# Performance work log

Hardware: AMD Instinct MI355X
Metric: run time of the kernel (lower is better)

## Reference

```python
import jax, jax.numpy as jnp
import numpy as np

B, T_ENC, T_DEC = 32, 512, 500
D_ENC = 512
N_MEL = 80 * 2  # mel_channels * mel_scale
K = 31          # location conv kernel size


def setup_inputs() -> dict:
    key = jax.random.key(0)
    ks = jax.random.split(key, 16)
    def w(k, shape, s=0.05):
        return jax.random.normal(k, shape, jnp.float32) * s
    z = lambda n: jnp.zeros((n,), jnp.float32)
    return {
        "encoder_out": w(ks[0], (B, T_ENC, D_ENC), 1.0),
        "mels": w(ks[1], (B, T_DEC, N_MEL), 1.0),
        "mask": jnp.zeros((B, 1, T_ENC), jnp.bool_),
        "w_pre1": w(ks[2], (256, N_MEL)), "b_pre1": z(256),
        "w_pre2": w(ks[3], (256, 256)), "b_pre2": z(256),
        "wih_a": w(ks[4], (4096, 256 + 512)), "whh_a": w(ks[5], (4096, 1024)),
        "bih_a": z(4096), "bhh_a": z(4096),
        "wq": w(ks[6], (128, 1024)), "bq": z(128),
        "wk": w(ks[7], (128, 512)), "bk": z(128),
        "conv_w": w(ks[8], (32, 2, K)), "conv_b": z(32),
        "wl": w(ks[9], (128, 32)), "bl": z(128),
        "wa": w(ks[10], (1, 128)), "ba": z(1),
        "wih_d": w(ks[11], (4096, 512 + 1024)), "whh_d": w(ks[12], (4096, 1024)),
        "bih_d": z(4096), "bhh_d": z(4096),
        "wm": w(ks[13], (N_MEL, 512 + 1024)), "bm": z(N_MEL),
        "wg": w(ks[14], (1, 512 + 1024)), "bg": z(1),
    }


def _lstm_cell(x, h, c, wih, whh, bih, bhh):
    g = x @ wih.T + bih + h @ whh.T + bhh
    i, f, gg, o = jnp.split(g, 4, axis=-1)
    c = jax.nn.sigmoid(f) * c + jax.nn.sigmoid(i) * jnp.tanh(gg)
    return jax.nn.sigmoid(o) * jnp.tanh(c), c


def _forward(encoder_out, mels, mask, w_pre1, b_pre1, w_pre2, b_pre2,
             wih_a, whh_a, bih_a, bhh_a, wq, bq, wk, bk, conv_w, conv_b,
             wl, bl, wa, ba, wih_d, whh_d, bih_d, bhh_d, wm, bm, wg, bg):
    b, t_enc, _ = encoder_out.shape
    n_mel = mels.shape[-1]
    mask1 = mask[:, 0, :]  # [B, T_enc], True = masked out
    # prepend zero frame, run prenet (ReLU MLP) over all frames at once
    mel_seq = jnp.concatenate([jnp.zeros((b, 1, n_mel), mels.dtype), mels], 1)
    pre = jax.nn.relu(mel_seq @ w_pre1.T + b_pre1)
    pre = jax.nn.relu(pre @ w_pre2.T + b_pre2)        # [B, T_dec+1, 256]
    pre = pre.transpose(1, 0, 2)                      # [T_dec+1, B, 256]
    mem_keys = encoder_out @ wk.T + bk                # [B, T_enc, 128]
    pad = K // 2

    def step(carry, mel_t):
        ctx, ah, ac, aw, awt, dh, dc = carry
        ah, ac = _lstm_cell(jnp.concatenate([mel_t, ctx], -1), ah, ac,
                            wih_a, whh_a, bih_a, bhh_a)
        query = ah @ wq.T + bq                        # [B, 128]
        fmap = jnp.stack([aw, awt], axis=1)           # [B, 2, T_enc]
        loc = jax.lax.conv_general_dilated(
            fmap, conv_w, (1,), [(pad, pad)],
            dimension_numbers=("NCH", "OIH", "NCH")) + conv_b[None, :, None]
        loc = loc.transpose(0, 2, 1) @ wl.T + bl      # [B, T_enc, 128]
        e = jnp.tanh(query[:, None, :] + mem_keys + loc) @ wa.T + ba  # [B,T_enc,1]
        e = jnp.where(mask1, -jnp.inf, e[..., 0])
        aw = jax.nn.softmax(e, -1)                    # [B, T_enc]
        awt = awt + aw
        ctx = jnp.einsum("bt,btd->bd", aw, encoder_out)
        dh, dc = _lstm_cell(jnp.concatenate([ctx, ah], -1), dh, dc,
                            wih_d, whh_d, bih_d, bhh_d)
        h = jnp.concatenate([dh, ctx], -1)            # [B, 1536]
        return (ctx, ah, ac, aw, awt, dh, dc), (h @ wm.T + bm, h @ wg.T + bg, aw)

    zf = lambda *s: jnp.zeros(s, encoder_out.dtype)
    carry0 = (zf(b, 512), zf(b, 1024), zf(b, 1024), zf(b, t_enc), zf(b, t_enc),
              zf(b, 1024), zf(b, 1024))
    _, (mels_out, gates_out, attn_out) = jax.lax.scan(step, carry0, pre)
    # mels_out [T_dec+1,B,n_mel], gates_out [T_dec+1,B,1], attn_out [T_dec+1,B,T_enc]
    return mels_out, gates_out, attn_out


def reference(encoder_out, mels, mask, w_pre1, b_pre1, w_pre2, b_pre2,
              wih_a, whh_a, bih_a, bhh_a, wq, bq, wk, bk, conv_w, conv_b,
              wl, bl, wa, ba, wih_d, whh_d, bih_d, bhh_d, wm, bm, wg, bg):
    return _forward(encoder_out, mels, mask, w_pre1, b_pre1, w_pre2, b_pre2,
                    wih_a, whh_a, bih_a, bhh_a, wq, bq, wk, bk, conv_w, conv_b,
                    wl, bl, wa, ba, wih_d, whh_d, bih_d, bhh_d, wm, bm, wg, bg)
```

## Files before the change

kernel.cpp:

```cpp
#include <hip/hip_runtime.h>
#include <hip/hip_bf16.h>


typedef __hip_bfloat16 bf16;

__device__ __forceinline__ float b2f(bf16 x){ return __bfloat162float(x); }
__device__ __forceinline__ bf16 f2b(float x){ return __float2bfloat16(x); }
__device__ __forceinline__ unsigned short f2bu(float x){
  union { bf16 h; unsigned short u; } cv; cv.h = __float2bfloat16(x); return cv.u;
}
__device__ __forceinline__ float us2f(unsigned short u){
  return __uint_as_float(((unsigned)u) << 16);
}
__device__ __forceinline__ float sig_s(float x){
  if (x > 30.f) return 1.f; if (x < -30.f) return 0.f;
  return 1.f/(1.f+__expf(-x)); }
__device__ __forceinline__ float tanh_s(float x){
  if (x > 15.f) return 1.f; if (x < -15.f) return -1.f;
  float e=__expf(2.f*x); return 1.f-2.f/(e+1.f); }

__device__ __forceinline__ float ld_cv(const float* p){
  return __hip_atomic_load(p, __ATOMIC_RELAXED, __HIP_MEMORY_SCOPE_AGENT);
}
__device__ __forceinline__ void st_cv(float* p, float v){
  __hip_atomic_store(p, v, __ATOMIC_RELAXED, __HIP_MEMORY_SCOPE_AGENT);
}

constexpr size_t S_MKT   = 32ull*128*512;
constexpr size_t OFF_MKT = 0;
constexpr size_t OFF_AC  = OFF_MKT + S_MKT;
constexpr size_t OFF_DC  = OFF_AC + 32*1024;
constexpr size_t OFF_AW  = OFF_DC + 32*1024;
constexpr size_t OFF_AWT = OFF_AW + 32*512;
constexpr size_t OFF_BARS= OFF_AWT + 32*512;
constexpr size_t OFF_XA  = OFF_BARS + 3072;
constexpr size_t ZERO_LEN = OFF_XA - OFF_AC;
constexpr size_t OFF_XD  = OFF_XA + 32*1792;
constexpr size_t OFF_GP  = OFF_XD + 32*2560;
constexpr size_t OFF_CNV = OFF_GP + 8ull*32*4096;
constexpr size_t OFF_RED = OFF_CNV + 32ull*32*512;
constexpr size_t OFF_BIASA = OFF_RED + 512;
constexpr size_t OFF_BIASD = OFF_BIASA + 4096;
constexpr size_t OFF_WQT   = OFF_BIASD + 4096;
constexpr size_t OFF_F32_END = OFF_WQT + 1024*128;

constexpr size_t OFF_PRE2B_BYTES = ((OFF_F32_END*4 + 255)/256)*256;
constexpr size_t S_PRE2B = 501ull*32*256;
constexpr size_t OFF_WAT_BYTES = ((OFF_PRE2B_BYTES + S_PRE2B*2 + 255)/256)*256;
constexpr size_t S_WAT = 1792ull*4096;
constexpr size_t OFF_WDT_BYTES = OFF_WAT_BYTES + S_WAT*2;
constexpr size_t S_WDT = 2560ull*4096;
constexpr size_t WS_NEEDED = OFF_WDT_BYTES + S_WDT*2;

constexpr int LDS_WA = 57344;
constexpr int LDS_WD = 81920;
constexpr int LDS_SCR = 23552;
constexpr int SMEM_TOTAL = LDS_WA + LDS_WD + LDS_SCR;

constexpr size_t OUT_MEL  = 0;
constexpr size_t OUT_GATE = 501ull*32*160;
constexpr size_t OUT_ATTN = OUT_GATE + 501ull*32;

__global__ void k_zero(float* __restrict__ p, int n){
  int i = blockIdx.x*256 + threadIdx.x;
  if (i < n) p[i] = 0.f;
}

__global__ void k_bias(const float* __restrict__ b1, const float* __restrict__ b2,
                       float* __restrict__ out){
  int i = blockIdx.x*256 + threadIdx.x;
  if (i < 4096) out[i] = b1[i] + b2[i];
}

__global__ __launch_bounds__(256) void k_wqT(const float* __restrict__ wq,
                                             float* __restrict__ wqT){
  int idx = blockIdx.x*256 + threadIdx.x;
  int k = idx >> 7, c = idx & 127;
  wqT[idx] = wq[(size_t)c*1024 + k];
}

__global__ __launch_bounds__(256) void k_trans(const float* __restrict__ src, int C,
    unsigned short* __restrict__ dst, int koff, int CH, int SLICE){
  __shared__ unsigned short tile[64][65];
  int r0 = blockIdx.x*64, c0 = blockIdx.y*64;
  int tx = threadIdx.x & 63, ty = threadIdx.x >> 6;
  for (int rr = ty; rr < 64; rr += 4)
    tile[rr][tx] = f2bu(src[(size_t)(r0+rr)*C + c0 + tx]);
  __syncthreads();
  for (int rr = ty; rr < 64; rr += 4){
    int k = koff + c0 + rr;
    int kcc = k / CH, kl = k - kcc*CH;
    int j = r0 + tx, jtt = j >> 7, jl = j & 127;
    dst[(size_t)(kcc*32 + jtt)*SLICE + (size_t)(kl >> 2)*512 + jl*4 + (kl & 3)] = tile[tx][rr];
  }
}

__global__ __launch_bounds__(256) void k_prenet(const float* __restrict__ mels,
    const float* __restrict__ w1, const float* __restrict__ b1,
    const float* __restrict__ w2, const float* __restrict__ b2,
    bf16* __restrict__ pre2){
  __shared__ float mel[160];
  __shared__ float x1[256];
  int b = blockIdx.x, tid = threadIdx.x;
  for (int ti = 0; ti < 8; ++ti){
    int tt = blockIdx.y*8 + ti;
    if (tt >= 501) break;
    if (tid < 160) mel[tid] = (tt == 0) ? 0.f : mels[((size_t)b*500 + (tt-1))*160 + tid];
    __syncthreads();
    float a = b1[tid];
    for (int k = 0; k < 160; ++k) a += mel[k]*w1[tid*160 + k];
    x1[tid] = fmaxf(a, 0.f);
    __syncthreads();
    float a2 = b2[tid];
    for (int k = 0; k < 256; ++k) a2 += x1[k]*w2[tid*256 + k];
    pre2[((size_t)tt*32 + b)*256 + tid] = f2b(fmaxf(a2, 0.f));
    __syncthreads();
  }
}

__global__ __launch_bounds__(128) void k_memkeys(const float* __restrict__ enc,
    const float* __restrict__ wk, const float* __restrict__ bk, float* __restrict__ mkT){
  __shared__ float er[512];
  int b = blockIdx.x, tid = threadIdx.x;
  for (int i = 0; i < 8; ++i){
    int t = blockIdx.y*8 + i;
    const float* e = enc + ((size_t)b*512 + t)*512;
    for (int k = tid; k < 512; k += 128) er[k] = e[k];
    __syncthreads();
    float a = bk[tid];
    for (int k = 0; k < 512; ++k) a += er[k]*wk[tid*512 + k];
    mkT[((size_t)b*128 + tid)*512 + t] = a;
    __syncthreads();
  }
}

__device__ __forceinline__ void gridbar(unsigned* cnt){
  asm volatile("s_waitcnt vmcnt(0) lgkmcnt(0)" ::: "memory");
  __syncthreads();
  if (threadIdx.x == 0){
    __hip_atomic_fetch_add(cnt, 1u, __ATOMIC_RELAXED, __HIP_MEMORY_SCOPE_AGENT);
    while (__hip_atomic_load(cnt, __ATOMIC_RELAXED, __HIP_MEMORY_SCOPE_AGENT) < 256u)
      __builtin_amdgcn_s_sleep(16);
  }
  __syncthreads();
}

template<int CH, int KS, int HK>
__device__ __forceinline__ void gates_phase(const unsigned short* __restrict__ smW,
    float* __restrict__ xs, const float* __restrict__ xcat,
    float* __restrict__ Gp, int jt, int kc, int tid){
  const int jl = tid & 127, bg = tid >> 7;
  float acc[8];
  #pragma unroll
  for (int i = 0; i < 8; ++i) acc[i] = 0.f;
  const int k0 = kc*CH;
  for (int h = 0; h < CH/HK; ++h){
    __syncthreads();
    for (int i = tid; i < 32*HK; i += 512){
      int b = i / HK, kk = i - b*HK;
      xs[i] = ld_cv(xcat + (size_t)b*KS + k0 + h*HK + kk);
    }
    __syncthreads();
    for (int kk = 0; kk < HK; kk += 4){
      const ushort4 w4 = *(const ushort4*)(smW + (size_t)((h*HK + kk) >> 2)*512 + jl*4);
      const float w0 = us2f(w4.x), w1 = us2f(w4.y), w2 = us2f(w4.z), w3 = us2f(w4.w);
      #pragma unroll
      for (int bb = 0; bb < 8; ++bb){
        const float4 xv = *(const float4*)&xs[(bg*8 + bb)*HK + kk];
        acc[bb] = fmaf(xv.x, w0, acc[bb]);
        acc[bb] = fmaf(xv.y, w1, acc[bb]);
        acc[bb] = fmaf(xv.z, w2, acc[bb]);
        acc[bb] = fmaf(xv.w, w3, acc[bb]);
      }
    }
  }
  float* gp = Gp + (size_t)kc*131072 + (size_t)(bg*8)*4096 + jt*128 + jl;
  #pragma unroll
  for (int bb = 0; bb < 8; ++bb) st_cv(gp + (size_t)bb*4096, acc[bb]);
}

__device__ __forceinline__ void out_proj(int wid, int lane, int t,
    const float* __restrict__ xcatD, const float* __restrict__ wm,
    const float* __restrict__ bm, const float* __restrict__ wg,
    const float* __restrict__ bg,
    float* __restrict__ melOut, float* __restrict__ gateOut, int stride){
  for (int oidx = wid; oidx < 32*161; oidx += stride){
    int b = oidx / 161, jo = oidx - b*161;
    const float* wrow = (jo < 160) ? (wm + (size_t)jo*1536) : wg;
    const float* xd = xcatD + (size_t)b*2560;
    float a = 0.f;
    for (int k = lane; k < 1536; k += 64){
      float x = (k < 1024) ? ld_cv(xd + 1536 + k) : ld_cv(xd + (k - 1024));
      a = fmaf(x, wrow[k], a);
    }
    #pragma unroll
    for (int off = 32; off; off >>= 1) a += __shfl_down(a, off, 64);
    if (lane == 0){
      if (jo < 160) melOut[((size_t)t*32 + b)*160 + jo] = a + bm[jo];
      else gateOut[t*32 + b] = a + bg[0];
    }
  }
}

__global__ __launch_bounds__(512) void k_decoder(
    const unsigned short* __restrict__ WaT, const unsigned short* __restrict__ WdT,
    const float* __restrict__ biasA, const float* __restrict__ biasD,
    const bf16* __restrict__ pre2b, const float* __restrict__ mkT,
    const float* __restrict__ enc, const unsigned char* __restrict__ mask,
    const float* __restrict__ wqT, const float* __restrict__ wl,
    const float* __restrict__ bq, const float* __restrict__ bl,
    const float* __restrict__ wa, const float* __restrict__ ba,
    const float* __restrict__ conv_w, const float* __restrict__ conv_b,
    const float* __restrict__ wm, const float* __restrict__ bm,
    const float* __restrict__ wg, const float* __restrict__ bg,
    float* __restrict__ xcatA, float* __restrict__ xcatD,
    float* __restrict__ ac, float* __restrict__ dc,
    float* __restrict__ aw, float* __restrict__ awt,
    float* __restrict__ Gp, float* __restrict__ cnv,
    float* __restrict__ redG, unsigned* __restrict__ bars,
    float* __restrict__ melOut, float* __restrict__ gateOut, float* __restrict__ attnOut)
{
  extern __shared__ __align__(16) char sm[];
  unsigned short* smWa = (unsigned short*)sm;
  unsigned short* smWd = (unsigned short*)(sm + LDS_WA);
  char* scr = sm + LDS_WA + LDS_WD;
  float* xs   = (float*)scr;
  float* s0   = (float*)scr;
  float* s1   = (float*)(scr + 640);
  float* wlS  = (float*)scr;
  float* ahS  = (float*)(scr + 16384);
  float* qpP  = (float*)(scr + 20480);
  float* sqS  = (float*)(scr + 22528);
  float* eT   = (float*)(scr + 23040);
  float* sawL = (float*)(scr + 23296);

  const int blk = blockIdx.x, tid = threadIdx.x;
  const int lane = tid & 63, wv = tid >> 6;
  const int jt = blk & 31, kc = blk >> 5;

  {
    const ushort4* sa = (const ushort4*)(WaT + (size_t)(kc*32 + jt)*28672);
    ushort4* da = (ushort4*)smWa;
    for (int i = tid; i < 7168; i += 512) da[i] = sa[i];
    const ushort4* sd = (const ushort4*)(WdT + (size_t)(kc*32 + jt)*40960);
    ushort4* dd = (ushort4*)smWd;
    for (int i = tid; i < 10240; i += 512) dd[i] = sd[i];
  }
  for (int idx = blk*512 + tid; idx < 32*1792; idx += 131072){
    int b = idx / 1792, i = idx - b*1792;
    st_cv(xcatA + idx, (i < 256) ? b2f(pre2b[b*256 + i]) : 0.f);
  }
  for (int idx = blk*512 + tid; idx < 32*2560; idx += 131072) st_cv(xcatD + idx, 0.f);

  int bi = 0;
  gridbar(bars + bi); ++bi;

  for (int t = 0; t < 501; ++t){
    gates_phase<224, 1792, 112>(smWa, xs, xcatA, Gp, jt, kc, tid);
    gridbar(bars + bi); ++bi;

    if (blk < 64){
      int idx = blk*512 + tid, b = idx >> 10, u = idx & 1023;
      float gi = biasA[u], gf = biasA[1024+u], gg = biasA[2048+u], go = biasA[3072+u];
      #pragma unroll
      for (int ci = 0; ci < 8; ++ci){
        const float* p = Gp + (size_t)ci*131072 + (size_t)b*4096 + u;
        gi += ld_cv(p); gf += ld_cv(p+1024); gg += ld_cv(p+2048); go += ld_cv(p+3072);
      }
      float cp = ac[idx];
      float cn = sig_s(gf)*cp + sig_s(gi)*tanh_s(gg);
      float hh = sig_s(go)*tanh_s(cn);
      ac[idx] = cn;
      st_cv(xcatA + (size_t)b*1792 + 768 + u, hh);
      st_cv(xcatD + (size_t)b*2560 + 512 + u, hh);
    } else if (blk < 128){
      if (t > 0)
        out_proj((blk-64)*8 + wv, lane, t-1, xcatD, wm, bm, wg, bg, melOut, gateOut, 512);
    } else {
      int cb = blk - 128, b = cb >> 2, tc = cb & 3, tbase = tc*128;
      for (int i = tid; i < 316; i += 512){
        int ch = (i >= 158), p2 = ch ? i-158 : i;
        int pos = tbase + p2 - 15;
        float v = (pos >= 0 && pos < 512)
                ? (ch ? ld_cv(awt + b*512 + pos) : ld_cv(aw + b*512 + pos)) : 0.f;
        if (ch) s1[p2] = v; else s0[p2] = v;
      }
      __syncthreads();
      int tt2 = tid & 127, oh = tid >> 7;
      float acc[8];
      #pragma unroll
      for (int o = 0; o < 8; ++o) acc[o] = 0.f;
      for (int k = 0; k < 31; ++k){
        float v0 = s0[tt2+k], v1 = s1[tt2+k];
        #pragma unroll
        for (int o = 0; o < 8; ++o){
          int oo = oh*8 + o;
          acc[o] = fmaf(conv_w[oo*62 + k], v0, fmaf(conv_w[oo*62 + 31 + k], v1, acc[o]));
        }
      }
      int tg = tbase + tt2;
      #pragma unroll
      for (int o = 0; o < 8; ++o){
        int oo = oh*8 + o;
        st_cv(cnv + ((size_t)b*32 + oo)*512 + tg, acc[o] + conv_b[oo]);
      }
    }
    gridbar(bars + bi); ++bi;

    {
      int b = blk >> 3, tt = blk & 7, t0 = tt*64;
      if (tid < 64){
        st_cv(xcatA + (size_t)b*1792 + 256 + t0 + tid, 0.f);
        st_cv(xcatD + (size_t)b*2560 + t0 + tid, 0.f);
      }
      for (int i = tid; i < 4096; i += 512) wlS[i] = wl[i];
      for (int i = tid; i < 1024; i += 512) ahS[i] = ld_cv(xcatA + (size_t)b*1792 + 768 + i);
      __syncthreads();
      {
        int c = tid & 127, kq = tid >> 7;
        const float* ap = ahS + kq*256;
        const float* wp = wqT + (size_t)(kq*256)*128 + c;
        float p = 0.f;
        for (int k = 0; k < 256; ++k) p = fmaf(ap[k], wp[(size_t)k*128], p);
        qpP[kq*128 + c] = p;
      }
      __syncthreads();
      if (tid < 128)
        sqS[tid] = qpP[tid] + qpP[128+tid] + qpP[256+tid] + qpP[384+tid] + bq[tid] + bl[tid];
      __syncthreads();
      int tl = tid & 63, cg = tid >> 6;
      float rv[32];
      {
        const float* cp2 = cnv + (size_t)b*32*512 + t0 + tl;
        #pragma unroll
        for (int o = 0; o < 32; ++o) rv[o] = ld_cv(cp2 + (size_t)o*512);
      }
      float a = 0.f;
      const float* mkb = mkT + (size_t)b*65536 + t0 + tl;
      for (int ci = 0; ci < 16; ++ci){
        int c = cg*16 + ci;
        const float* wr = wlS + c*32;
        float lc = 0.f;
        #pragma unroll
        for (int o = 0; o < 32; ++o) lc = fmaf(wr[o], rv[o], lc);
        float s = sqS[c] + mkb[(size_t)c*512] + lc;
        a = fmaf(tanh_s(s), wa[c], a);
      }
      qpP[cg*64 + tl] = a;
      __syncthreads();
      if (tid < 64){
        float e = ba[0];
        #pragma unroll
        for (int g = 0; g < 8; ++g) e += qpP[g*64 + tid];
        if (mask[b*512 + t0 + tid]) e = -1e30f;
        eT[tid] = e;
        float m = e;
        #pragma unroll
        for (int off = 32; off; off >>= 1) m = fmaxf(m, __shfl_xor(m, off, 64));
        float pe = __expf(e - m), ss = pe;
        #pragma unroll
        for (int off = 32; off; off >>= 1) ss += __shfl_xor(ss, off, 64);
        if (tid == 0){
          st_cv(redG + (size_t)(b*8 + tt)*2, m);
          st_cv(redG + (size_t)(b*8 + tt)*2 + 1, ss);
        }
      }
    }
    gridbar(bars + bi); ++bi;

    {
      int b = blk >> 3, tt = blk & 7, t0 = tt*64;
      if (tid < 64){
        float mi[8], si[8], M = -1e30f, S = 0.f;
        #pragma unroll
        for (int i = 0; i < 8; ++i){
          mi[i] = ld_cv(redG + (size_t)(b*8 + i)*2);
          si[i] = ld_cv(redG + (size_t)(b*8 + i)*2 + 1);
          M = fmaxf(M, mi[i]);
        }
        #pragma unroll
        for (int i = 0; i < 8; ++i) S += si[i]*__expf(mi[i] - M);
        float av = __expf(eT[tid] - M)/S;
        int tg = t0 + tid;
        st_cv(aw + b*512 + tg, av);
        st_cv(awt + b*512 + tg, ld_cv(awt + b*512 + tg) + av);
        attnOut[((size_t)t*32 + b)*512 + tg] = av;
        sawL[tid] = av;
      }
      __syncthreads();
      {
        float accd = 0.f;
        const float* eb = enc + ((size_t)b*512 + t0)*512 + tid;
        for (int tau = 0; tau < 64; ++tau) accd = fmaf(sawL[tau], eb[(size_t)tau*512], accd);
        __hip_atomic_fetch_add(xcatA + (size_t)b*1792 + 256 + tid, accd,
                               __ATOMIC_RELAXED, __HIP_MEMORY_SCOPE_AGENT);
        __hip_atomic_fetch_add(xcatD + (size_t)b*2560 + tid, accd,
                               __ATOMIC_RELAXED, __HIP_MEMORY_SCOPE_AGENT);
      }
    }
    gridbar(bars + bi); ++bi;

    gates_phase<320, 2560, 160>(smWd, xs, xcatD, Gp, jt, kc, tid);
    gridbar(bars + bi); ++bi;

    if (blk < 64){
      int idx = blk*512 + tid, b = idx >> 10, u = idx & 1023;
      float gi = biasD[u], gf = biasD[1024+u], gg = biasD[2048+u], go = biasD[3072+u];
      #pragma unroll
      for (int ci = 0; ci < 8; ++ci){
        const float* p = Gp + (size_t)ci*131072 + (size_t)b*4096 + u;
        gi += ld_cv(p); gf += ld_cv(p+1024); gg += ld_cv(p+2048); go += ld_cv(p+3072);
      }
      float cp = dc[idx];
      float cn = sig_s(gf)*cp + sig_s(gi)*tanh_s(gg);
      float hh = sig_s(go)*tanh_s(cn);
      dc[idx] = cn;
      st_cv(xcatD + (size_t)b*2560 + 1536 + u, hh);
    } else if (blk < 96){
      if (t < 500){
        int b = blk - 64;
        for (int i = tid; i < 256; i += 512)
          st_cv(xcatA + (size_t)b*1792 + i, b2f(pre2b[((size_t)(t+1)*32 + b)*256 + i]));
      }
    }
    gridbar(bars + bi); ++bi;
  }

  out_proj(blk*8 + wv, lane, 500, xcatD, wm, bm, wg, bg, melOut, gateOut, 2048);
}

extern "C" void kernel_launch(void* const* d_in, const int* in_sizes, int n_in,
                              void* d_out, int out_size, void* d_ws, size_t ws_size,
                              hipStream_t stream){
  if (ws_size < WS_NEEDED) return;

  const float* enc    = (const float*)d_in[0];
  const float* mels   = (const float*)d_in[1];
  const unsigned char* mask = (const unsigned char*)d_in[2];
  const float* w_pre1 = (const float*)d_in[3];
  const float* b_pre1 = (const float*)d_in[4];
  const float* w_pre2 = (const float*)d_in[5];
  const float* b_pre2 = (const float*)d_in[6];
  const float* wih_a  = (const float*)d_in[7];
  const float* whh_a  = (const float*)d_in[8];
  const float* bih_a  = (const float*)d_in[9];
  const float* bhh_a  = (const float*)d_in[10];
  const float* wq     = (const float*)d_in[11];
  const float* bq     = (const float*)d_in[12];
  const float* wk     = (const float*)d_in[13];
  const float* bk     = (const float*)d_in[14];
  const float* conv_w = (const float*)d_in[15];
  const float* conv_b = (const float*)d_in[16];
  const float* wl     = (const float*)d_in[17];
  const float* bl     = (const float*)d_in[18];
  const float* wa     = (const float*)d_in[19];
  const float* ba     = (const float*)d_in[20];
  const float* wih_d  = (const float*)d_in[21];
  const float* whh_d  = (const float*)d_in[22];
  const float* bih_d  = (const float*)d_in[23];
  const float* bhh_d  = (const float*)d_in[24];
  const float* wm     = (const float*)d_in[25];
  const float* bm     = (const float*)d_in[26];
  const float* wg     = (const float*)d_in[27];
  const float* bg     = (const float*)d_in[28];

  float* W = (float*)d_ws;
  float* mkT   = W + OFF_MKT;
  float* ac    = W + OFF_AC;
  float* dc    = W + OFF_DC;
  float* aw    = W + OFF_AW;
  float* awt   = W + OFF_AWT;
  unsigned* bars = (unsigned*)(W + OFF_BARS);
  float* xcatA = W + OFF_XA;
  float* xcatD = W + OFF_XD;
  float* Gp    = W + OFF_GP;
  float* cnv   = W + OFF_CNV;
  float* redG  = W + OFF_RED;
  float* biasA = W + OFF_BIASA;
  float* biasD = W + OFF_BIASD;
  float* wqT   = W + OFF_WQT;
  unsigned short* WaT = (unsigned short*)((char*)d_ws + OFF_WAT_BYTES);
  unsigned short* WdT = (unsigned short*)((char*)d_ws + OFF_WDT_BYTES);
  bf16* pre2b = (bf16*)((char*)d_ws + OFF_PRE2B_BYTES);

  float* out    = (float*)d_out;
  float* melOut = out + OUT_MEL;
  float* gateOut= out + OUT_GATE;
  float* attnOut= out + OUT_ATTN;

  static int smem_set = 0;
  if (!smem_set){
    hipFuncSetAttribute((const void*)k_decoder,
                        hipFuncAttributeMaxDynamicSharedMemorySize, SMEM_TOTAL);
    smem_set = 1;
  }

  k_zero<<<(int)((ZERO_LEN + 255)/256), 256, 0, stream>>>(W + OFF_AC, (int)ZERO_LEN);
  k_bias<<<16, 256, 0, stream>>>(bih_a, bhh_a, biasA);
  k_bias<<<16, 256, 0, stream>>>(bih_d, bhh_d, biasD);
  k_wqT<<<512, 256, 0, stream>>>(wq, wqT);
  k_trans<<<dim3(64, 12), 256, 0, stream>>>(wih_a, 768,  WaT, 0,    224, 28672);
  k_trans<<<dim3(64, 16), 256, 0, stream>>>(whh_a, 1024, WaT, 768,  224, 28672);
  k_trans<<<dim3(64, 24), 256, 0, stream>>>(wih_d, 1536, WdT, 0,    320, 40960);
  k_trans<<<dim3(64, 16), 256, 0, stream>>>(whh_d, 1024, WdT, 1536, 320, 40960);
  k_prenet<<<dim3(32, 63), 256, 0, stream>>>(mels, w_pre1, b_pre1, w_pre2, b_pre2, pre2b);
  k_memkeys<<<dim3(32, 64), 128, 0, stream>>>(enc, wk, bk, mkT);

  k_decoder<<<256, 512, SMEM_TOTAL, stream>>>(WaT, WdT, biasA, biasD, pre2b, mkT, enc, mask,
                                              wqT, wl, bq, bl, wa, ba, conv_w, conv_b,
                                              wm, bm, wg, bg, xcatA, xcatD, ac, dc, aw, awt,
                                              Gp, cnv, redG, bars, melOut, gateOut, attnOut);
}
```

Baseline: 137.9 ms.

## Fold location conv into projection, vectorize coherent loads, restructure per-step phases

Precomputes a fused weight combining the location conv kernel with the location projection, so the conv phase writes 128-channel location features directly and the attention-energy phase no longer does a 32x128 matmul per step. Also vectorizes coherent global loads and stores into 64-bit pairs, halves the number of blocks doing LSTM cell updates with two units per thread, stages decoder hidden state in LDS for the output projection with one block per batch, and shortens the barrier sleep. The conv phase now does more FLOPs (128 output channels instead of 32) and needs a larger workspace buffer, trading that for less work in the energy phase.

```diff
diff --git a/kernel.cpp b/kernel.cpp
--- a/kernel.cpp
+++ b/kernel.cpp
@@ -24,6 +24,15 @@
 }
 __device__ __forceinline__ void st_cv(float* p, float v){
   __hip_atomic_store(p, v, __ATOMIC_RELAXED, __HIP_MEMORY_SCOPE_AGENT);
+}
+__device__ __forceinline__ float2 ld_cv2(const float* p){
+  union { double d; float2 f; } u;
+  u.d = __hip_atomic_load((const double*)p, __ATOMIC_RELAXED, __HIP_MEMORY_SCOPE_AGENT);
+  return u.f;
+}
+__device__ __forceinline__ void st_cv2(float* p, float2 v){
+  union { double d; float2 f; } u; u.f = v;
+  __hip_atomic_store((double*)p, u.d, __ATOMIC_RELAXED, __HIP_MEMORY_SCOPE_AGENT);
 }
 
 constexpr size_t S_MKT   = 32ull*128*512;
@@ -37,11 +46,13 @@
 constexpr size_t ZERO_LEN = OFF_XA - OFF_AC;
 constexpr size_t OFF_XD  = OFF_XA + 32*1792;
 constexpr size_t OFF_GP  = OFF_XD + 32*2560;
-constexpr size_t OFF_CNV = OFF_GP + 8ull*32*4096;
-constexpr size_t OFF_RED = OFF_CNV + 32ull*32*512;
+constexpr size_t OFF_LOC = OFF_GP + 8ull*32*4096;
+constexpr size_t OFF_RED = OFF_LOC + 32ull*128*512;
 constexpr size_t OFF_BIASA = OFF_RED + 512;
 constexpr size_t OFF_BIASD = OFF_BIASA + 4096;
-constexpr size_t OFF_WQT   = OFF_BIASD + 4096;
+constexpr size_t OFF_WFOLD = OFF_BIASD + 4096;
+constexpr size_t OFF_QBIAS = OFF_WFOLD + 7936;
+constexpr size_t OFF_WQT   = OFF_QBIAS + 128;
 constexpr size_t OFF_F32_END = OFF_WQT + 1024*128;
 
 constexpr size_t OFF_PRE2B_BYTES = ((OFF_F32_END*4 + 255)/256)*256;
@@ -70,6 +81,21 @@
                        float* __restrict__ out){
   int i = blockIdx.x*256 + threadIdx.x;
   if (i < 4096) out[i] = b1[i] + b2[i];
+}
+
+__global__ void k_fold(const float* __restrict__ cw, const float* __restrict__ cb,
+                       const float* __restrict__ wl, const float* __restrict__ bl,
+                       const float* __restrict__ bq,
+                       float* __restrict__ wfold, float* __restrict__ qbias){
+  int c = threadIdx.x;
+  for (int kk = 0; kk < 62; ++kk){
+    float a = 0.f;
+    for (int o = 0; o < 32; ++o) a += wl[c*32 + o]*cw[o*62 + kk];
+    wfold[c*62 + kk] = a;
+  }
+  float q = bq[c] + bl[c];
+  for (int o = 0; o < 32; ++o) q += wl[c*32 + o]*cb[o];
+  qbias[c] = q;
 }
 
 __global__ __launch_bounds__(256) void k_wqT(const float* __restrict__ wq,
@@ -140,7 +166,7 @@
   if (threadIdx.x == 0){
     __hip_atomic_fetch_add(cnt, 1u, __ATOMIC_RELAXED, __HIP_MEMORY_SCOPE_AGENT);
     while (__hip_atomic_load(cnt, __ATOMIC_RELAXED, __HIP_MEMORY_SCOPE_AGENT) < 256u)
-      __builtin_amdgcn_s_sleep(16);
+      __builtin_amdgcn_s_sleep(8);
   }
   __syncthreads();
 }
@@ -156,9 +182,9 @@
   const int k0 = kc*CH;
   for (int h = 0; h < CH/HK; ++h){
     __syncthreads();
-    for (int i = tid; i < 32*HK; i += 512){
-      int b = i / HK, kk = i - b*HK;
-      xs[i] = ld_cv(xcat + (size_t)b*KS + k0 + h*HK + kk);
+    for (int i = tid; i < 16*HK; i += 512){
+      int b = i/(HK/2), kp = i - b*(HK/2);
+      ((float2*)xs)[i] = ld_cv2(xcat + (size_t)b*KS + k0 + h*HK + 2*kp);
     }
     __syncthreads();
     for (int kk = 0; kk < HK; kk += 4){
@@ -179,18 +205,46 @@
   for (int bb = 0; bb < 8; ++bb) st_cv(gp + (size_t)bb*4096, acc[bb]);
 }
 
-__device__ __forceinline__ void out_proj(int wid, int lane, int t,
+__device__ __forceinline__ void cell_phase(const float* __restrict__ Gp,
+    const float* __restrict__ bias, float* __restrict__ cst,
+    float* __restrict__ h0, int h0stride, int h0off,
+    float* __restrict__ h1, int h1stride, int h1off,
+    int blk, int tid){
+  int idx = (blk*512 + tid)*2;
+  int b = idx >> 10, u = idx & 1023;
+  float gi0 = bias[u],      gi1 = bias[u+1];
+  float gf0 = bias[1024+u], gf1 = bias[1024+u+1];
+  float gg0 = bias[2048+u], gg1 = bias[2048+u+1];
+  float go0 = bias[3072+u], go1 = bias[3072+u+1];
+  #pragma unroll
+  for (int ci = 0; ci < 8; ++ci){
+    const float* p = Gp + (size_t)ci*131072 + (size_t)b*4096 + u;
+    float2 a = ld_cv2(p), f = ld_cv2(p+1024), g = ld_cv2(p+2048), o = ld_cv2(p+3072);
+    gi0 += a.x; gi1 += a.y; gf0 += f.x; gf1 += f.y;
+    gg0 += g.x; gg1 += g.y; go0 += o.x; go1 += o.y;
+  }
+  float2 cp = *(const float2*)(cst + idx);
+  float cn0 = sig_s(gf0)*cp.x + sig_s(gi0)*tanh_s(gg0);
+  float cn1 = sig_s(gf1)*cp.y + sig_s(gi1)*tanh_s(gg1);
+  float2 hh = make_float2(sig_s(go0)*tanh_s(cn0), sig_s(go1)*tanh_s(cn1));
+  *(float2*)(cst + idx) = make_float2(cn0, cn1);
+  st_cv2(h0 + (size_t)b*h0stride + h0off + u, hh);
+  if (h1) st_cv2(h1 + (size_t)b*h1stride + h1off + u, hh);
+}
+
+__device__ __forceinline__ void out_proj_b(int b, int tid, int lane, int wv, int t,
     const float* __restrict__ xcatD, const float* __restrict__ wm,
     const float* __restrict__ bm, const float* __restrict__ wg,
     const float* __restrict__ bg,
-    float* __restrict__ melOut, float* __restrict__ gateOut, int stride){
-  for (int oidx = wid; oidx < 32*161; oidx += stride){
-    int b = oidx / 161, jo = oidx - b*161;
+    float* __restrict__ melOut, float* __restrict__ gateOut, float* __restrict__ xdS){
+  for (int i = tid; i < 1280; i += 512)
+    ((float2*)xdS)[i] = ld_cv2(xcatD + (size_t)b*2560 + 2*i);
+  __syncthreads();
+  for (int jo = wv; jo < 161; jo += 8){
     const float* wrow = (jo < 160) ? (wm + (size_t)jo*1536) : wg;
-    const float* xd = xcatD + (size_t)b*2560;
     float a = 0.f;
     for (int k = lane; k < 1536; k += 64){
-      float x = (k < 1024) ? ld_cv(xd + 1536 + k) : ld_cv(xd + (k - 1024));
+      float x = (k < 1024) ? xdS[1536 + k] : xdS[k - 1024];
       a = fmaf(x, wrow[k], a);
     }
     #pragma unroll
@@ -207,16 +261,15 @@
     const float* __restrict__ biasA, const float* __restrict__ biasD,
     const bf16* __restrict__ pre2b, const float* __restrict__ mkT,
     const float* __restrict__ enc, const unsigned char* __restrict__ mask,
-    const float* __restrict__ wqT, const float* __restrict__ wl,
-    const float* __restrict__ bq, const float* __restrict__ bl,
-    const float* __restrict__ wa, const float* __restrict__ ba,
-    const float* __restrict__ conv_w, const float* __restrict__ conv_b,
-    const float* __restrict__ wm, const float* __restrict__ bm,
-    const float* __restrict__ wg, const float* __restrict__ bg,
+    const float* __restrict__ wqT, const float* __restrict__ qbias,
+    const float* __restrict__ wfold, const float* __restrict__ wa,
+    const float* __restrict__ ba, const float* __restrict__ wm,
+    const float* __restrict__ bm, const float* __restrict__ wg,
+    const float* __restrict__ bg,
     float* __restrict__ xcatA, float* __restrict__ xcatD,
     float* __restrict__ ac, float* __restrict__ dc,
     float* __restrict__ aw, float* __restrict__ awt,
-    float* __restrict__ Gp, float* __restrict__ cnv,
+    float* __restrict__ Gp, float* __restrict__ loc,
     float* __restrict__ redG, unsigned* __restrict__ bars,
     float* __restrict__ melOut, float* __restrict__ gateOut, float* __restrict__ attnOut)
 {
@@ -227,7 +280,7 @@
   float* xs   = (float*)scr;
   float* s0   = (float*)scr;
   float* s1   = (float*)(scr + 640);
-  float* wlS  = (float*)scr;
+  float* xdS  = (float*)scr;
   float* ahS  = (float*)(scr + 16384);
   float* qpP  = (float*)(scr + 20480);
   float* sqS  = (float*)(scr + 22528);
@@ -259,24 +312,13 @@
     gates_phase<224, 1792, 112>(smWa, xs, xcatA, Gp, jt, kc, tid);
     gridbar(bars + bi); ++bi;
 
-    if (blk < 64){
-      int idx = blk*512 + tid, b = idx >> 10, u = idx & 1023;
-      float gi = biasA[u], gf = biasA[1024+u], gg = biasA[2048+u], go = biasA[3072+u];
-      #pragma unroll
-      for (int ci = 0; ci < 8; ++ci){
-        const float* p = Gp + (size_t)ci*131072 + (size_t)b*4096 + u;
-        gi += ld_cv(p); gf += ld_cv(p+1024); gg += ld_cv(p+2048); go += ld_cv(p+3072);
-      }
-      float cp = ac[idx];
-      float cn = sig_s(gf)*cp + sig_s(gi)*tanh_s(gg);
-      float hh = sig_s(go)*tanh_s(cn);
-      ac[idx] = cn;
-      st_cv(xcatA + (size_t)b*1792 + 768 + u, hh);
-      st_cv(xcatD + (size_t)b*2560 + 512 + u, hh);
-    } else if (blk < 128){
+    if (blk < 32){
+      cell_phase(Gp, biasA, ac, xcatA, 1792, 768, xcatD, 2560, 512, blk, tid);
+    } else if (blk >= 64 && blk < 96){
       if (t > 0)
-        out_proj((blk-64)*8 + wv, lane, t-1, xcatD, wm, bm, wg, bg, melOut, gateOut, 512);
-    } else {
+        out_proj_b(blk-64, tid, lane, wv, t-1, xcatD, wm, bm, wg, bg,
+                   melOut, gateOut, xdS);
+    } else if (blk >= 128){
       int cb = blk - 128, b = cb >> 2, tc = cb & 3, tbase = tc*128;
       for (int i = tid; i < 316; i += 512){
         int ch = (i >= 158), p2 = ch ? i-158 : i;
@@ -286,35 +328,29 @@
         if (ch) s1[p2] = v; else s0[p2] = v;
       }
       __syncthreads();
-      int tt2 = tid & 127, oh = tid >> 7;
-      float acc[8];
-      #pragma unroll
-      for (int o = 0; o < 8; ++o) acc[o] = 0.f;
-      for (int k = 0; k < 31; ++k){
-        float v0 = s0[tt2+k], v1 = s1[tt2+k];
+      int tt2 = tid & 127, cg = tid >> 7;
+      int tg = tbase + tt2;
+      for (int ci = 0; ci < 32; ++ci){
+        int c = cg*32 + ci;
+        const float* wfr = wfold + c*62;
+        float a = 0.f;
         #pragma unroll
-        for (int o = 0; o < 8; ++o){
-          int oo = oh*8 + o;
-          acc[o] = fmaf(conv_w[oo*62 + k], v0, fmaf(conv_w[oo*62 + 31 + k], v1, acc[o]));
-        }
-      }
-      int tg = tbase + tt2;
-      #pragma unroll
-      for (int o = 0; o < 8; ++o){
-        int oo = oh*8 + o;
-        st_cv(cnv + ((size_t)b*32 + oo)*512 + tg, acc[o] + conv_b[oo]);
+        for (int k = 0; k < 31; ++k)
+          a = fmaf(wfr[k], s0[tt2+k], fmaf(wfr[31+k], s1[tt2+k], a));
+        st_cv(loc + ((size_t)b*128 + c)*512 + tg, a);
       }
     }
     gridbar(bars + bi); ++bi;
 
     {
       int b = blk >> 3, tt = blk & 7, t0 = tt*64;
-      if (tid < 64){
-        st_cv(xcatA + (size_t)b*1792 + 256 + t0 + tid, 0.f);
-        st_cv(xcatD + (size_t)b*2560 + t0 + tid, 0.f);
-      }
-      for (int i = tid; i < 4096; i += 512) wlS[i] = wl[i];
-      for (int i = tid; i < 1024; i += 512) ahS[i] = ld_cv(xcatA + (size_t)b*1792 + 768 + i);
+      if (tid < 32){
+        float2 z = make_float2(0.f, 0.f);
+        st_cv2(xcatA + (size_t)b*1792 + 256 + t0 + 2*tid, z);
+        st_cv2(xcatD + (size_t)b*2560 + t0 + 2*tid, z);
+      }
+      for (int i = tid; i < 512; i += 512)
+        ((float2*)ahS)[i] = ld_cv2(xcatA + (size_t)b*1792 + 768 + 2*i);
       __syncthreads();
       {
         int c = tid & 127, kq = tid >> 7;
@@ -326,24 +362,15 @@
       }
       __syncthreads();
       if (tid < 128)
-        sqS[tid] = qpP[tid] + qpP[128+tid] + qpP[256+tid] + qpP[384+tid] + bq[tid] + bl[tid];
+        sqS[tid] = qpP[tid] + qpP[128+tid] + qpP[256+tid] + qpP[384+tid] + qbias[tid];
       __syncthreads();
       int tl = tid & 63, cg = tid >> 6;
-      float rv[32];
-      {
-        const float* cp2 = cnv + (size_t)b*32*512 + t0 + tl;
-        #pragma unroll
-        for (int o = 0; o < 32; ++o) rv[o] = ld_cv(cp2 + (size_t)o*512);
-      }
       float a = 0.f;
       const float* mkb = mkT + (size_t)b*65536 + t0 + tl;
+      const float* lcb = loc + (size_t)b*65536 + t0 + tl;
       for (int ci = 0; ci < 16; ++ci){
         int c = cg*16 + ci;
-        const float* wr = wlS + c*32;
-        float lc = 0.f;
-        #pragma unroll
-        for (int o = 0; o < 32; ++o) lc = fmaf(wr[o], rv[o], lc);
-        float s = sqS[c] + mkb[(size_t)c*512] + lc;
+        float s = sqS[c] + mkb[(size_t)c*512] + ld_cv(lcb + (size_t)c*512);
         a = fmaf(tanh_s(s), wa[c], a);
       }
       qpP[cg*64 + tl] = a;
@@ -361,8 +388,7 @@
         #pragma unroll
         for (int off = 32; off; off >>= 1) ss += __shfl_xor(ss, off, 64);
         if (tid == 0){
-          st_cv(redG + (size_t)(b*8 + tt)*2, m);
-          st_cv(redG + (size_t)(b*8 + tt)*2 + 1, ss);
+          st_cv2(redG + (size_t)(b*8 + tt)*2, make_float2(m, ss));
         }
       }
     }
@@ -371,15 +397,15 @@
     {
       int b = blk >> 3, tt = blk & 7, t0 = tt*64;
       if (tid < 64){
-        float mi[8], si[8], M = -1e30f, S = 0.f;
+        float M = -1e30f, S = 0.f;
+        float2 ms[8];
         #pragma unroll
         for (int i = 0; i < 8; ++i){
-          mi[i] = ld_cv(redG + (size_t)(b*8 + i)*2);
-          si[i] = ld_cv(redG + (size_t)(b*8 + i)*2 + 1);
-          M = fmaxf(M, mi[i]);
+          ms[i] = ld_cv2(redG + (size_t)(b*8 + i)*2);
+          M = fmaxf(M, ms[i].x);
         }
         #pragma unroll
-        for (int i = 0; i < 8; ++i) S += si[i]*__expf(mi[i] - M);
+        for (int i = 0; i < 8; ++i) S += ms[i].y*__expf(ms[i].x - M);
         float av = __expf(eT[tid] - M)/S;
         int tg = t0 + tid;
         st_cv(aw + b*512 + tg, av);
@@ -403,30 +429,22 @@
     gates_phase<320, 2560, 160>(smWd, xs, xcatD, Gp, jt, kc, tid);
     gridbar(bars + bi); ++bi;
 
-    if (blk < 64){
-      int idx = blk*512 + tid, b = idx >> 10, u = idx & 1023;
-      float gi = biasD[u], gf = biasD[1024+u], gg = biasD[2048+u], go = biasD[3072+u];
-      #pragma unroll
-      for (int ci = 0; ci < 8; ++ci){
-        const float* p = Gp + (size_t)ci*131072 + (size_t)b*4096 + u;
-        gi += ld_cv(p); gf += ld_cv(p+1024); gg += ld_cv(p+2048); go += ld_cv(p+3072);
-      }
-      float cp = dc[idx];
-      float cn = sig_s(gf)*cp + sig_s(gi)*tanh_s(gg);
-      float hh = sig_s(go)*tanh_s(cn);
-      dc[idx] = cn;
-      st_cv(xcatD + (size_t)b*2560 + 1536 + u, hh);
-    } else if (blk < 96){
+    if (blk < 32){
+      cell_phase(Gp, biasD, dc, xcatD, 2560, 1536, nullptr, 0, 0, blk, tid);
+    } else if (blk < 64){
       if (t < 500){
-        int b = blk - 64;
-        for (int i = tid; i < 256; i += 512)
-          st_cv(xcatA + (size_t)b*1792 + i, b2f(pre2b[((size_t)(t+1)*32 + b)*256 + i]));
+        int b = blk - 32;
+        const bf16* ps = pre2b + ((size_t)(t+1)*32 + b)*256;
+        for (int i = tid; i < 128; i += 512)
+          st_cv2(xcatA + (size_t)b*1792 + 2*i,
+                 make_float2(b2f(ps[2*i]), b2f(ps[2*i+1])));
       }
     }
     gridbar(bars + bi); ++bi;
   }
 
-  out_proj(blk*8 + wv, lane, 500, xcatD, wm, bm, wg, bg, melOut, gateOut, 2048);
+  if (blk < 32)
+    out_proj_b(blk, tid, lane, wv, 500, xcatD, wm, bm, wg, bg, melOut, gateOut, xdS);
 }
 
 extern "C" void kernel_launch(void* const* d_in, const int* in_sizes, int n_in,
@@ -474,10 +492,12 @@
   float* xcatA = W + OFF_XA;
   float* xcatD = W + OFF_XD;
   float* Gp    = W + OFF_GP;
-  float* cnv   = W + OFF_CNV;
+  float* loc   = W + OFF_LOC;
   float* redG  = W + OFF_RED;
   float* biasA = W + OFF_BIASA;
   float* biasD = W + OFF_BIASD;
+  float* wfold = W + OFF_WFOLD;
+  float* qbias = W + OFF_QBIAS;
   float* wqT   = W + OFF_WQT;
   unsigned short* WaT = (unsigned short*)((char*)d_ws + OFF_WAT_BYTES);
   unsigned short* WdT = (unsigned short*)((char*)d_ws + OFF_WDT_BYTES);
@@ -498,6 +518,7 @@
   k_zero<<<(int)((ZERO_LEN + 255)/256), 256, 0, stream>>>(W + OFF_AC, (int)ZERO_LEN);
   k_bias<<<16, 256, 0, stream>>>(bih_a, bhh_a, biasA);
   k_bias<<<16, 256, 0, stream>>>(bih_d, bhh_d, biasD);
+  k_fold<<<1, 128, 0, stream>>>(conv_w, conv_b, wl, bl, bq, wfold, qbias);
   k_wqT<<<512, 256, 0, stream>>>(wq, wqT);
   k_trans<<<dim3(64, 12), 256, 0, stream>>>(wih_a, 768,  WaT, 0,    224, 28672);
   k_trans<<<dim3(64, 16), 256, 0, stream>>>(whh_a, 1024, WaT, 768,  224, 28672);
@@ -507,7 +528,8 @@
   k_memkeys<<<dim3(32, 64), 128, 0, stream>>>(enc, wk, bk, mkT);
 
   k_decoder<<<256, 512, SMEM_TOTAL, stream>>>(WaT, WdT, biasA, biasD, pre2b, mkT, enc, mask,
-                                              wqT, wl, bq, bl, wa, ba, conv_w, conv_b,
-                                              wm, bm, wg, bg, xcatA, xcatD, ac, dc, aw, awt,
-                                              Gp, cnv, redG, bars, melOut, gateOut, attnOut);
-}
+                                              wqT, qbias, wfold, wa, ba, wm, bm, wg, bg,
+                                              xcatA, xcatD, ac, dc, aw, awt,
+                                              Gp, loc, redG, bars,
+                                              melOut, gateOut, attnOut);
+}
```

Measured after the change: 174.3 ms. 26.4% more time.
